# Kernel optimization log

Measured on AMD Instinct MI355X. Metric: run time of the kernel, lower is better.

The kernel has to match this reference:

```python
import jax, jax.numpy as jnp
import numpy as np

N, E, G = 100000, 1600000, 64
FIN, D, OUT = 4, 64, 16
EPS = 1e-5


def _lin(key, fi, fo):
    kw, kb = jax.random.split(key)
    w = jax.random.normal(kw, (fi, fo), dtype=jnp.float32) / np.sqrt(fi)
    b = jnp.zeros((fo,), dtype=jnp.float32)
    return w, b


def setup_inputs() -> dict:
    key = jax.random.key(0)
    ks = jax.random.split(key, 24)
    inp = {}
    inp['h'] = jax.random.normal(ks[0], (N, FIN), dtype=jnp.float32)
    inp['pos'] = jax.random.normal(ks[1], (N, 3), dtype=jnp.float32)
    inp['edge_index'] = jax.random.randint(ks[2], (2, E), 0, N, dtype=jnp.int32)
    inp['batch'] = jnp.sort(jax.random.randint(ks[3], (N,), 0, G, dtype=jnp.int32))
    inp['fe_w'], inp['fe_b'] = _lin(ks[4], FIN, D)
    i = 5
    for c in ('c1', 'c2'):
        inp[c + 'h_w1'], inp[c + 'h_b1'] = _lin(ks[i], D, D); i += 1
        inp[c + 'h_w2'], inp[c + 'h_b2'] = _lin(ks[i], D, 3); i += 1
        inp[c + 'f_w1'], inp[c + 'f_b1'] = _lin(ks[i], D + 3, D); i += 1
        inp[c + 'f_w2'], inp[c + 'f_b2'] = _lin(ks[i], D, D); i += 1
        inp[c + 'g_w1'], inp[c + 'g_b1'] = _lin(ks[i], D, D); i += 1
        inp[c + 'g_gm'] = jnp.ones((D,), dtype=jnp.float32)
        inp[c + 'g_bt'] = jnp.zeros((D,), dtype=jnp.float32)
        inp[c + 'g_w2'], inp[c + 'g_b2'] = _lin(ks[i], D, D); i += 1
    inp['ro_w1'], inp['ro_b1'] = _lin(ks[i], D, D); i += 1
    inp['ro_w2'], inp['ro_b2'] = _lin(ks[i], D, OUT)
    return inp


def _mlp2(x, w1, b1, w2, b2):
    return jnp.maximum(x @ w1 + b1, 0.0) @ w2 + b2


def _bn(x, gm, bt):
    # BatchNorm1d in training mode: batch stats over the node axis
    m = jnp.mean(x, axis=0)
    v = jnp.var(x, axis=0)
    return (x - m) * jax.lax.rsqrt(v + EPS) * gm + bt


def _pointgnn_conv(x, pos, src, dst, hw1, hb1, hw2, hb2, fw1, fb1, fw2, fb2,
                   gw1, gb1, ggm, gbt, gw2, gb2):
    delta = _mlp2(x, hw1, hb1, hw2, hb2)                      # [N,3]
    rel = pos[src] - pos[dst] + delta[dst]                    # [E,3]
    msg = _mlp2(jnp.concatenate([rel, x[src]], axis=-1), fw1, fb1, fw2, fb2)  # [E,D]
    agg = jax.ops.segment_max(msg, dst, num_segments=x.shape[0])
    agg = jnp.where(jnp.isneginf(agg), 0.0, agg)              # empty segments -> 0
    g = jnp.maximum(agg @ gw1 + gb1, 0.0)
    g = _bn(g, ggm, gbt)
    return x + (g @ gw2 + gb2)


def reference(h, pos, edge_index, batch, fe_w, fe_b,
              c1h_w1, c1h_b1, c1h_w2, c1h_b2, c1f_w1, c1f_b1, c1f_w2, c1f_b2,
              c1g_w1, c1g_b1, c1g_gm, c1g_bt, c1g_w2, c1g_b2,
              c2h_w1, c2h_b1, c2h_w2, c2h_b2, c2f_w1, c2f_b1, c2f_w2, c2f_b2,
              c2g_w1, c2g_b1, c2g_gm, c2g_bt, c2g_w2, c2g_b2,
              ro_w1, ro_b1, ro_w2, ro_b2):
    src, dst = edge_index[0], edge_index[1]
    x = h @ fe_w + fe_b
    x = _pointgnn_conv(x, pos, src, dst, c1h_w1, c1h_b1, c1h_w2, c1h_b2,
                       c1f_w1, c1f_b1, c1f_w2, c1f_b2,
                       c1g_w1, c1g_b1, c1g_gm, c1g_bt, c1g_w2, c1g_b2)
    x = _pointgnn_conv(x, pos, src, dst, c2h_w1, c2h_b1, c2h_w2, c2h_b2,
                       c2f_w1, c2f_b1, c2f_w2, c2f_b2,
                       c2g_w1, c2g_b1, c2g_gm, c2g_bt, c2g_w2, c2g_b2)
    # global mean pool over graphs
    sums = jax.ops.segment_sum(x, batch, num_segments=G)
    cnts = jax.ops.segment_sum(jnp.ones((x.shape[0], 1), x.dtype), batch, num_segments=G)
    pooled = sums / jnp.maximum(cnts, 1.0)
    return _mlp2(pooled, ro_w1, ro_b1, ro_w2, ro_b2)
```

## Files before the change

### kernel.cpp

```cpp
#include <hip/hip_runtime.h>

#define NN 100000
#define NE 1600000
#define NG 64
#define EPS 1e-5f
#define SCAN_NB 98

#define FOR16(M) M(0) M(1) M(2) M(3) M(4) M(5) M(6) M(7) M(8) M(9) M(10) M(11) M(12) M(13) M(14) M(15)

#define WDECL(i) float4 wr##i##_;
#define LDW(i, RB, P) \
  wr##i##_.x = (P)[((RB) + 4 * i + 0) * 64 + lane]; \
  wr##i##_.y = (P)[((RB) + 4 * i + 1) * 64 + lane]; \
  wr##i##_.z = (P)[((RB) + 4 * i + 2) * 64 + lane]; \
  wr##i##_.w = (P)[((RB) + 4 * i + 3) * 64 + lane];
#define WPIN(i) asm volatile("" : "+v"(wr##i##_.x), "+v"(wr##i##_.y), "+v"(wr##i##_.z), "+v"(wr##i##_.w));
#define DOTR(i) { float4 v = xr[i]; \
  a0 = fmaf(v.x, wr##i##_.x, a0); a1 = fmaf(v.y, wr##i##_.y, a1); \
  a2 = fmaf(v.z, wr##i##_.z, a2); a3 = fmaf(v.w, wr##i##_.w, a3); }
#define DOTB(i, SRC) { \
  a0 = fmaf(bcast(SRC, 4 * i + 0), wr##i##_.x, a0); \
  a1 = fmaf(bcast(SRC, 4 * i + 1), wr##i##_.y, a1); \
  a2 = fmaf(bcast(SRC, 4 * i + 2), wr##i##_.z, a2); \
  a3 = fmaf(bcast(SRC, 4 * i + 3), wr##i##_.w, a3); }

#define BDECL(i) float4 br##i##_;
#define LDB(i, RB, P) \
  br##i##_.x = (P)[((RB) + 4 * i + 0) * 64 + lane]; \
  br##i##_.y = (P)[((RB) + 4 * i + 1) * 64 + lane]; \
  br##i##_.z = (P)[((RB) + 4 * i + 2) * 64 + lane]; \
  br##i##_.w = (P)[((RB) + 4 * i + 3) * 64 + lane];
#define BPIN(i) asm volatile("" : "+v"(br##i##_.x), "+v"(br##i##_.y), "+v"(br##i##_.z), "+v"(br##i##_.w));
#define DOTRB(i) { float4 v = xr[i]; \
  a0 = fmaf(v.x, br##i##_.x, a0); a1 = fmaf(v.y, br##i##_.y, a1); \
  a2 = fmaf(v.z, br##i##_.z, a2); a3 = fmaf(v.w, br##i##_.w, a3); }

__device__ __forceinline__ int wave_gid() {
  return __builtin_amdgcn_readfirstlane((int)((blockIdx.x * blockDim.x + threadIdx.x) >> 6));
}

__device__ __forceinline__ float bcast(float v, int l) {
  return __uint_as_float(__builtin_amdgcn_readlane(__float_as_uint(v), l));
}

__device__ __forceinline__ void graph_range(const int* __restrict__ batch, int g, int& s, int& e) {
  int a = 0, b = NN;
  while (a < b) { int m = (a + b) >> 1; if (batch[m] < g) a = m + 1; else b = m; }
  s = a;
  b = NN;
  while (a < b) { int m = (a + b) >> 1; if (batch[m] < g + 1) a = m + 1; else b = m; }
  e = a;
}

__global__ void k_zero(unsigned* __restrict__ hist, float* __restrict__ psum) {
  int i = blockIdx.x * blockDim.x + threadIdx.x;
  int st = gridDim.x * blockDim.x;
  for (int j = i; j < NN; j += st) hist[j] = 0u;
  for (int j = i; j < NG * 64; j += st) psum[j] = 0.f;
}

__global__ void k_hist(const int* __restrict__ ei, unsigned* __restrict__ hist) {
  int i = blockIdx.x * blockDim.x + threadIdx.x;
  int st = gridDim.x * blockDim.x;
  for (int e = i; e < NE; e += st) atomicAdd(&hist[ei[NE + e]], 1u);
}

__global__ void k_scan1(const unsigned* __restrict__ hist, unsigned* __restrict__ coff,
                        unsigned* __restrict__ bsum) {
  __shared__ unsigned sd[256];
  int t = threadIdx.x;
  int base = blockIdx.x * 1024 + t * 4;
  unsigned v0 = (base + 0 < NN) ? hist[base + 0] : 0u;
  unsigned v1 = (base + 1 < NN) ? hist[base + 1] : 0u;
  unsigned v2 = (base + 2 < NN) ? hist[base + 2] : 0u;
  unsigned v3 = (base + 3 < NN) ? hist[base + 3] : 0u;
  unsigned tsum = v0 + v1 + v2 + v3;
  sd[t] = tsum;
  __syncthreads();
  for (int off = 1; off < 256; off <<= 1) {
    unsigned add = (t >= off) ? sd[t - off] : 0u;
    __syncthreads();
    sd[t] += add;
    __syncthreads();
  }
  unsigned p = sd[t] - tsum;
  if (t == 255) bsum[blockIdx.x] = sd[255];
  if (base + 0 < NN) coff[base + 0] = p; p += v0;
  if (base + 1 < NN) coff[base + 1] = p; p += v1;
  if (base + 2 < NN) coff[base + 2] = p; p += v2;
  if (base + 3 < NN) coff[base + 3] = p;
}

__global__ void k_scan2(unsigned* __restrict__ bsum) {
  __shared__ unsigned sd[128];
  int t = threadIdx.x;
  unsigned v = (t < SCAN_NB) ? bsum[t] : 0u;
  sd[t] = v;
  __syncthreads();
  for (int off = 1; off < 128; off <<= 1) {
    unsigned add = (t >= off) ? sd[t - off] : 0u;
    __syncthreads();
    sd[t] += add;
    __syncthreads();
  }
  if (t < SCAN_NB) bsum[t] = sd[t] - v;
}

__global__ void k_scan3(unsigned* __restrict__ coff, const unsigned* __restrict__ bsum,
                        unsigned* __restrict__ cursor) {
  int i = blockIdx.x * blockDim.x + threadIdx.x;
  if (i < NN) {
    unsigned v = coff[i] + bsum[i >> 10];
    coff[i] = v;
    cursor[i] = v;
  }
  if (i == 0) coff[NN] = NE;
}

__global__ void k_scatter(const int* __restrict__ ei, unsigned* __restrict__ cursor,
                          int* __restrict__ csrc) {
  int i = blockIdx.x * blockDim.x + threadIdx.x;
  int st = gridDim.x * blockDim.x;
  for (int e = i; e < NE; e += st) {
    int dst = ei[NE + e];
    unsigned p = atomicAdd(&cursor[dst], 1u);
    csrc[p] = ei[e];
  }
}

__global__ void __launch_bounds__(256) k_init_x(const float* __restrict__ h,
                                                const float* __restrict__ few,
                                                const float* __restrict__ feb,
                                                float* __restrict__ x) {
  int lane = threadIdx.x & 63;
  int wg = wave_gid();
  int nw = (gridDim.x * blockDim.x) >> 6;
  float c0 = few[0 * 64 + lane], c1 = few[1 * 64 + lane];
  float c2 = few[2 * 64 + lane], c3 = few[3 * 64 + lane];
  float b = feb[lane];
  for (int n = wg; n < NN; n += nw) {
    float4 hv = *(const float4*)(h + (size_t)n * 4);
    x[(size_t)n * 64 + lane] = fmaf(hv.x, c0, fmaf(hv.y, c1, fmaf(hv.z, c2, fmaf(hv.w, c3, b))));
  }
}

__global__ void __launch_bounds__(256) k_node_pre(
    const float* __restrict__ x, const float* __restrict__ pos,
    const float* __restrict__ hw1, const float* __restrict__ hb1,
    const float* __restrict__ hw2, const float* __restrict__ hb2,
    const float* __restrict__ fw1, const float* __restrict__ fb1,
    float* __restrict__ q, float* __restrict__ xa) {
  int lane = threadIdx.x & 63;
  int wg = wave_gid();
  int nw = (gridDim.x * blockDim.x) >> 6;
  FOR16(WDECL)
  FOR16(BDECL)
#define LD(i) LDW(i, 0, hw1)
  FOR16(LD)
#undef LD
#define LD(i) LDB(i, 3, fw1)
  FOR16(LD)
#undef LD
  FOR16(WPIN)
  FOR16(BPIN)
  float b1 = hb1[lane];
  float fb = fb1[lane];
  float u0 = hw2[lane * 3 + 0], u1 = hw2[lane * 3 + 1], u2 = hw2[lane * 3 + 2];
  float b20 = hb2[0], b21 = hb2[1], b22 = hb2[2];
  for (int n = wg; n < NN; n += nw) {
    const float4* xr = (const float4*)(x + (size_t)n * 64);
    float a0 = 0.f, a1 = 0.f, a2 = 0.f, a3 = 0.f;
    FOR16(DOTR)
    float t = fmaxf((a0 + a1) + (a2 + a3) + b1, 0.f);
    float p0 = t * u0, p1 = t * u1, p2 = t * u2;
#pragma unroll
    for (int off = 32; off; off >>= 1) {
      p0 += __shfl_xor(p0, off);
      p1 += __shfl_xor(p1, off);
      p2 += __shfl_xor(p2, off);
    }
    a0 = 0.f; a1 = 0.f; a2 = 0.f; a3 = 0.f;
    FOR16(DOTRB)
    xa[(size_t)n * 64 + lane] = (a0 + a1) + (a2 + a3) + fb;
    if (lane < 3) {
      float dc = (lane == 0) ? (p0 + b20) : ((lane == 1) ? (p1 + b21) : (p2 + b22));
      q[(size_t)n * 4 + lane] = pos[(size_t)n * 3 + lane] - dc;
    }
  }
}

__global__ void __launch_bounds__(256) k_edge_csr(
    const float* __restrict__ xa, const float* __restrict__ pos,
    const float* __restrict__ q, const unsigned* __restrict__ coff,
    const int* __restrict__ csrc, const float* __restrict__ fw1,
    const float* __restrict__ fb2_, const float* __restrict__ fw2,
    float* __restrict__ agg) {
  int lane = threadIdx.x & 63;
  int wg = wave_gid();
  int nw = (gridDim.x * blockDim.x) >> 6;
  FOR16(WDECL)
#define LD(i) LDW(i, 0, fw2)
  FOR16(LD)
#undef LD
  FOR16(WPIN)
  float pw0 = fw1[0 * 64 + lane], pw1 = fw1[1 * 64 + lane], pw2 = fw1[2 * 64 + lane];
  float bl = fb2_[lane];
  const float NEGINF = __int_as_float(0xff800000);
  for (int dst = wg; dst < NN; dst += nw) {
    unsigned s = coff[dst], e = coff[dst + 1];
    float4 qd = *(const float4*)(q + (size_t)dst * 4);
    float mx = NEGINF;
    if (e > s) {
      int src = csrc[s];
      float px = pos[(size_t)src * 3 + 0];
      float py = pos[(size_t)src * 3 + 1];
      float pz = pos[(size_t)src * 3 + 2];
      float hh = xa[(size_t)src * 64 + lane];
      for (unsigned i = s; i < e; ++i) {
        float cpx = px, cpy = py, cpz = pz, chh = hh;
        if (i + 1 < e) {
          int ns = csrc[i + 1];
          px = pos[(size_t)ns * 3 + 0];
          py = pos[(size_t)ns * 3 + 1];
          pz = pos[(size_t)ns * 3 + 2];
          hh = xa[(size_t)ns * 64 + lane];
        }
        float rx = cpx - qd.x, ry = cpy - qd.y, rz = cpz - qd.z;
        float pre = fmaxf(fmaf(rx, pw0, fmaf(ry, pw1, fmaf(rz, pw2, chh))), 0.f);
        float a0 = bl, a1 = 0.f, a2 = 0.f, a3 = 0.f;
#define DB(i) DOTB(i, pre)
        FOR16(DB)
#undef DB
        mx = fmaxf(mx, (a0 + a1) + (a2 + a3));
      }
    }
    agg[(size_t)dst * 64 + lane] = (e > s) ? mx : 0.f;
  }
}

__global__ void __launch_bounds__(256) k_g_bn(
    const float* __restrict__ agg, const float* __restrict__ gw1,
    const float* __restrict__ gb1, float* __restrict__ g, float* __restrict__ bnp) {
  __shared__ float2 red[4][64];
  int lane = threadIdx.x & 63;
  int wid = threadIdx.x >> 6;
  int wg = wave_gid();
  int nw = (gridDim.x * blockDim.x) >> 6;
  FOR16(WDECL)
#define LD(i) LDW(i, 0, gw1)
  FOR16(LD)
#undef LD
  FOR16(WPIN)
  float b = gb1[lane];
  float s = 0.f, ss = 0.f;
  for (int n = wg; n < NN; n += nw) {
    float av = agg[(size_t)n * 64 + lane];
    float a0 = 0.f, a1 = 0.f, a2 = 0.f, a3 = 0.f;
#define DB(i) DOTB(i, av)
    FOR16(DB)
#undef DB
    float gv = fmaxf((a0 + a1) + (a2 + a3) + b, 0.f);
    g[(size_t)n * 64 + lane] = gv;
    s += gv;
    ss += gv * gv;
  }
  red[wid][lane] = make_float2(s, ss);
  __syncthreads();
  if (wid == 0) {
    float2 r0 = red[0][lane], r1 = red[1][lane], r2 = red[2][lane], r3 = red[3][lane];
    bnp[(size_t)blockIdx.x * 128 + lane] = r0.x + r1.x + r2.x + r3.x;
    bnp[(size_t)blockIdx.x * 128 + 64 + lane] = r0.y + r1.y + r2.y + r3.y;
  }
}

#define NBLK_BN 256
__global__ void k_bn_final(const float* __restrict__ bnp, const float* __restrict__ gm,
                           const float* __restrict__ bt, const float* __restrict__ gw2,
                           const float* __restrict__ gb2, float* __restrict__ w2p,
                           float* __restrict__ b2p) {
  __shared__ float sums[128];
  __shared__ float sc[64], sh[64];
  int t = threadIdx.x;
  int c = t & 63;
  int kind = t >> 6;
  float acc = 0.f;
#pragma unroll 8
  for (int bId = 0; bId < NBLK_BN; ++bId) acc += bnp[(size_t)bId * 128 + kind * 64 + c];
  sums[t] = acc;
  __syncthreads();
  if (t < 64) {
    float mean = sums[t] * (1.f / (float)NN);
    float var = sums[64 + t] * (1.f / (float)NN) - mean * mean;
    float scale = gm[t] * rsqrtf(var + EPS);
    sc[t] = scale;
    sh[t] = bt[t] - mean * scale;
  }
  __syncthreads();
  for (int i = t; i < 4096; i += 128) {
    int d = i >> 6;
    w2p[i] = sc[d] * gw2[i];
  }
  if (t < 64) {
    float acc2 = gb2[t];
#pragma unroll 8
    for (int d = 0; d < 64; ++d) acc2 = fmaf(sh[d], gw2[d * 64 + t], acc2);
    b2p[t] = acc2;
  }
}

__global__ void __launch_bounds__(256) k_update(
    const float* __restrict__ g, const float* __restrict__ w2p,
    const float* __restrict__ b2p, float* __restrict__ x) {
  int lane = threadIdx.x & 63;
  int wg = wave_gid();
  int nw = (gridDim.x * blockDim.x) >> 6;
  FOR16(WDECL)
#define LD(i) LDW(i, 0, w2p)
  FOR16(LD)
#undef LD
  FOR16(WPIN)
  float b = b2p[lane];
  for (int n = wg; n < NN; n += nw) {
    const float4* xr = (const float4*)(g + (size_t)n * 64);
    float a0 = 0.f, a1 = 0.f, a2 = 0.f, a3 = 0.f;
    FOR16(DOTR)
    size_t idx = (size_t)n * 64 + lane;
    x[idx] = x[idx] + (a0 + a1) + (a2 + a3) + b;
  }
}

__global__ void __launch_bounds__(512) k_pool_partial(const float* __restrict__ x,
                                                      const int* __restrict__ batch,
                                                      float* __restrict__ psum) {
  __shared__ float red[8][64];
  int lane = threadIdx.x & 63;
  int wid = threadIdx.x >> 6;
  int g = blockIdx.x >> 2;
  int part = blockIdx.x & 3;
  int s, e;
  graph_range(batch, g, s, e);
  float acc = 0.f;
  for (int n = s + part * 8 + wid; n < e; n += 32) acc += x[(size_t)n * 64 + lane];
  red[wid][lane] = acc;
  __syncthreads();
  if (wid == 0) {
    float t = acc;
#pragma unroll
    for (int w = 1; w < 8; ++w) t += red[w][lane];
    atomicAdd(&psum[(size_t)g * 64 + lane], t);
  }
}

__global__ void __launch_bounds__(64) k_readout(
    const float* __restrict__ psum, const int* __restrict__ batch,
    const float* __restrict__ w1, const float* __restrict__ b1,
    const float* __restrict__ w2, const float* __restrict__ b2,
    float* __restrict__ out) {
  __shared__ float hs[64];
  int lane = threadIdx.x;
  int g = blockIdx.x;
  int s, e;
  graph_range(batch, g, s, e);
  float scale = 1.f / fmaxf((float)(e - s), 1.f);
  FOR16(WDECL)
#define LD(i) LDW(i, 0, w1)
  FOR16(LD)
#undef LD
  const float4* xr = (const float4*)(psum + (size_t)g * 64);
  float a0 = 0.f, a1 = 0.f, a2 = 0.f, a3 = 0.f;
  FOR16(DOTR)
  hs[lane] = fmaxf(((a0 + a1) + (a2 + a3)) * scale + b1[lane], 0.f);
  __syncthreads();
  if (lane < 16) {
    float acc = b2[lane];
#pragma unroll
    for (int l = 0; l < 64; ++l) acc = fmaf(hs[l], w2[l * 16 + lane], acc);
    out[(size_t)g * 16 + lane] = acc;
  }
}

extern "C" void kernel_launch(void* const* d_in, const int* in_sizes, int n_in,
                              void* d_out, int out_size, void* d_ws, size_t ws_size,
                              hipStream_t stream) {
  const float* h = (const float*)d_in[0];
  const float* pos = (const float*)d_in[1];
  const int* ei = (const int*)d_in[2];
  const int* batch = (const int*)d_in[3];
  const float* fe_w = (const float*)d_in[4];
  const float* fe_b = (const float*)d_in[5];
  const float* ro_w1 = (const float*)d_in[34];
  const float* ro_b1 = (const float*)d_in[35];
  const float* ro_w2 = (const float*)d_in[36];
  const float* ro_b2 = (const float*)d_in[37];
  float* out = (float*)d_out;

  char* ws = (char*)d_ws;
  const size_t SZ_ROW = (size_t)NN * 64 * sizeof(float);
  float* x = (float*)(ws); ws += SZ_ROW;
  float* xa = (float*)(ws); ws += SZ_ROW;
  float* agg = (float*)(ws); ws += SZ_ROW;
  float* q = (float*)(ws); ws += (size_t)NN * 4 * sizeof(float);
  float* bnp = (float*)(ws); ws += (size_t)NBLK_BN * 128 * sizeof(float);
  float* w2p = (float*)(ws); ws += 4096 * sizeof(float);
  float* b2p = (float*)(ws); ws += 256;
  float* psum = (float*)(ws); ws += (size_t)NG * 64 * sizeof(float);
  unsigned* cursor = (unsigned*)(ws); ws += ((size_t)NN * 4 + 256);
  unsigned* coff = (unsigned*)(ws); ws += ((size_t)(NN + 1) * 4 + 252);
  unsigned* bsum = (unsigned*)(ws); ws += 512;
  int* csrc = (int*)(ws); ws += (size_t)NE * 4;

  const int NB_NODE = 512;
  const int NB_EDGE = 4096;

  k_zero<<<256, 256, 0, stream>>>(cursor, psum);
  k_hist<<<1024, 256, 0, stream>>>(ei, cursor);
  k_scan1<<<SCAN_NB, 256, 0, stream>>>(cursor, coff, bsum);
  k_scan2<<<1, 128, 0, stream>>>(bsum);
  k_scan3<<<392, 256, 0, stream>>>(coff, bsum, cursor);
  k_scatter<<<1024, 256, 0, stream>>>(ei, cursor, csrc);

  k_init_x<<<NB_NODE, 256, 0, stream>>>(h, fe_w, fe_b, x);

  for (int layer = 0; layer < 2; ++layer) {
    int base = (layer == 0) ? 6 : 20;
    const float* hw1 = (const float*)d_in[base + 0];
    const float* hb1 = (const float*)d_in[base + 1];
    const float* hw2 = (const float*)d_in[base + 2];
    const float* hb2 = (const float*)d_in[base + 3];
    const float* fw1 = (const float*)d_in[base + 4];
    const float* fb1 = (const float*)d_in[base + 5];
    const float* fw2 = (const float*)d_in[base + 6];
    const float* fb2 = (const float*)d_in[base + 7];
    const float* gw1 = (const float*)d_in[base + 8];
    const float* gb1 = (const float*)d_in[base + 9];
    const float* ggm = (const float*)d_in[base + 10];
    const float* gbt = (const float*)d_in[base + 11];
    const float* gw2 = (const float*)d_in[base + 12];
    const float* gb2 = (const float*)d_in[base + 13];

    k_node_pre<<<NB_NODE, 256, 0, stream>>>(x, pos, hw1, hb1, hw2, hb2, fw1, fb1, q, xa);
    k_edge_csr<<<NB_EDGE, 256, 0, stream>>>(xa, pos, q, coff, csrc, fw1, fb2, fw2, agg);
    float* g = xa;
    k_g_bn<<<NBLK_BN, 256, 0, stream>>>(agg, gw1, gb1, g, bnp);
    k_bn_final<<<1, 128, 0, stream>>>(bnp, ggm, gbt, gw2, gb2, w2p, b2p);
    k_update<<<NB_NODE, 256, 0, stream>>>(g, w2p, b2p, x);
  }

  k_pool_partial<<<NG * 4, 512, 0, stream>>>(x, batch, psum);
  k_readout<<<NG, 64, 0, stream>>>(psum, batch, ro_w1, ro_b1, ro_w2, ro_b2, out);
}
```

Measured before the change: 1.373 ms.

## Stage edge pre-activations through LDS and pad positions to float4 in edge kernel

The edge kernel now computes the ReLU pre-activation for the next source one step early and writes it to a per-wave double-buffered LDS slot. The 64-wide dot product then reads it as float4 LDS loads instead of 64 readlane broadcasts. Positions are repacked once into a padded float4 array so each edge needs one vector load instead of three scalar loads. A launch-bounds occupancy hint and a sched barrier are also added. Without explicit wave barriers, the LDS round trip relies on wave-level lockstep for correctness.

```diff
diff --git a/kernel.cpp b/kernel.cpp
--- a/kernel.cpp
+++ b/kernel.cpp
@@ -23,6 +23,9 @@
   a1 = fmaf(bcast(SRC, 4 * i + 1), wr##i##_.y, a1); \
   a2 = fmaf(bcast(SRC, 4 * i + 2), wr##i##_.z, a2); \
   a3 = fmaf(bcast(SRC, 4 * i + 3), wr##i##_.w, a3); }
+#define DOTL(i) { float4 hv = hr[i]; \
+  a0 = fmaf(hv.x, wr##i##_.x, a0); a1 = fmaf(hv.y, wr##i##_.y, a1); \
+  a2 = fmaf(hv.z, wr##i##_.z, a2); a3 = fmaf(hv.w, wr##i##_.w, a3); }
 
 #define BDECL(i) float4 br##i##_;
 #define LDB(i, RB, P) \
@@ -52,10 +55,15 @@
   e = a;
 }
 
-__global__ void k_zero(unsigned* __restrict__ hist, float* __restrict__ psum) {
+__global__ void k_zero(unsigned* __restrict__ hist, float* __restrict__ psum,
+                       const float* __restrict__ pos, float4* __restrict__ pos4) {
   int i = blockIdx.x * blockDim.x + threadIdx.x;
   int st = gridDim.x * blockDim.x;
-  for (int j = i; j < NN; j += st) hist[j] = 0u;
+  for (int j = i; j < NN; j += st) {
+    hist[j] = 0u;
+    pos4[j] = make_float4(pos[(size_t)j * 3 + 0], pos[(size_t)j * 3 + 1],
+                          pos[(size_t)j * 3 + 2], 0.f);
+  }
   for (int j = i; j < NG * 64; j += st) psum[j] = 0.f;
 }
 
@@ -189,13 +197,15 @@
   }
 }
 
-__global__ void __launch_bounds__(256) k_edge_csr(
-    const float* __restrict__ xa, const float* __restrict__ pos,
+__global__ void __launch_bounds__(256, 3) k_edge_csr(
+    const float* __restrict__ xa, const float4* __restrict__ pos4,
     const float* __restrict__ q, const unsigned* __restrict__ coff,
     const int* __restrict__ csrc, const float* __restrict__ fw1,
     const float* __restrict__ fb2_, const float* __restrict__ fw2,
     float* __restrict__ agg) {
-  int lane = threadIdx.x & 63;
+  __shared__ __align__(16) float hbuf[4][2][64];
+  int lane = threadIdx.x & 63;
+  int wid = threadIdx.x >> 6;
   int wg = wave_gid();
   int nw = (gridDim.x * blockDim.x) >> 6;
   FOR16(WDECL)
@@ -208,33 +218,40 @@
   const float NEGINF = __int_as_float(0xff800000);
   for (int dst = wg; dst < NN; dst += nw) {
     unsigned s = coff[dst], e = coff[dst + 1];
-    float4 qd = *(const float4*)(q + (size_t)dst * 4);
-    float mx = NEGINF;
+    float mx;
     if (e > s) {
+      float4 qd = *(const float4*)(q + (size_t)dst * 4);
       int src = csrc[s];
-      float px = pos[(size_t)src * 3 + 0];
-      float py = pos[(size_t)src * 3 + 1];
-      float pz = pos[(size_t)src * 3 + 2];
+      float4 ps = pos4[src];
       float hh = xa[(size_t)src * 64 + lane];
+      float pre = fmaxf(fmaf(ps.x - qd.x, pw0,
+                        fmaf(ps.y - qd.y, pw1,
+                        fmaf(ps.z - qd.z, pw2, hh))), 0.f);
+      hbuf[wid][0][lane] = pre;
+      int cur = 0;
+      mx = NEGINF;
       for (unsigned i = s; i < e; ++i) {
-        float cpx = px, cpy = py, cpz = pz, chh = hh;
         if (i + 1 < e) {
           int ns = csrc[i + 1];
-          px = pos[(size_t)ns * 3 + 0];
-          py = pos[(size_t)ns * 3 + 1];
-          pz = pos[(size_t)ns * 3 + 2];
-          hh = xa[(size_t)ns * 64 + lane];
+          float4 ps2 = pos4[ns];
+          float hh2 = xa[(size_t)ns * 64 + lane];
+          float pre2 = fmaxf(fmaf(ps2.x - qd.x, pw0,
+                             fmaf(ps2.y - qd.y, pw1,
+                             fmaf(ps2.z - qd.z, pw2, hh2))), 0.f);
+          hbuf[wid][cur ^ 1][lane] = pre2;
         }
-        float rx = cpx - qd.x, ry = cpy - qd.y, rz = cpz - qd.z;
-        float pre = fmaxf(fmaf(rx, pw0, fmaf(ry, pw1, fmaf(rz, pw2, chh))), 0.f);
+        const float4* hr = (const float4*)hbuf[wid][cur];
         float a0 = bl, a1 = 0.f, a2 = 0.f, a3 = 0.f;
-#define DB(i) DOTB(i, pre)
-        FOR16(DB)
-#undef DB
+        DOTL(0) DOTL(1) DOTL(2) DOTL(3) DOTL(4) DOTL(5) DOTL(6) DOTL(7)
+        __builtin_amdgcn_sched_barrier(0);
+        DOTL(8) DOTL(9) DOTL(10) DOTL(11) DOTL(12) DOTL(13) DOTL(14) DOTL(15)
         mx = fmaxf(mx, (a0 + a1) + (a2 + a3));
+        cur ^= 1;
       }
+    } else {
+      mx = 0.f;
     }
-    agg[(size_t)dst * 64 + lane] = (e > s) ? mx : 0.f;
+    agg[(size_t)dst * 64 + lane] = mx;
   }
 }
 
@@ -404,6 +421,7 @@
   float* w2p = (float*)(ws); ws += 4096 * sizeof(float);
   float* b2p = (float*)(ws); ws += 256;
   float* psum = (float*)(ws); ws += (size_t)NG * 64 * sizeof(float);
+  float4* pos4 = (float4*)(ws); ws += (size_t)NN * sizeof(float4);
   unsigned* cursor = (unsigned*)(ws); ws += ((size_t)NN * 4 + 256);
   unsigned* coff = (unsigned*)(ws); ws += ((size_t)(NN + 1) * 4 + 252);
   unsigned* bsum = (unsigned*)(ws); ws += 512;
@@ -412,7 +430,7 @@
   const int NB_NODE = 512;
   const int NB_EDGE = 4096;
 
-  k_zero<<<256, 256, 0, stream>>>(cursor, psum);
+  k_zero<<<256, 256, 0, stream>>>(cursor, psum, pos, pos4);
   k_hist<<<1024, 256, 0, stream>>>(ei, cursor);
   k_scan1<<<SCAN_NB, 256, 0, stream>>>(cursor, coff, bsum);
   k_scan2<<<1, 128, 0, stream>>>(bsum);
@@ -439,7 +457,7 @@
     const float* gb2 = (const float*)d_in[base + 13];
 
     k_node_pre<<<NB_NODE, 256, 0, stream>>>(x, pos, hw1, hb1, hw2, hb2, fw1, fb1, q, xa);
-    k_edge_csr<<<NB_EDGE, 256, 0, stream>>>(xa, pos, q, coff, csrc, fw1, fb2, fw2, agg);
+    k_edge_csr<<<NB_EDGE, 256, 0, stream>>>(xa, pos4, q, coff, csrc, fw1, fb2, fw2, agg);
     float* g = xa;
     k_g_bn<<<NBLK_BN, 256, 0, stream>>>(agg, gw1, gb1, g, bnp);
     k_bn_final<<<1, 128, 0, stream>>>(bnp, ggm, gbt, gw2, gb2, w2p, b2p);
```

New measurement: 1.434 ms. +4.5%, slower.
